# Optimization experiments

Hardware: AMD Instinct MI355X
Metric: run time of the kernel (lower is better)

Reference implementation:

```python
import jax, jax.numpy as jnp
import numpy as np

EPS = 1e-3

def setup_inputs() -> dict:
    key = jax.random.key(0)
    k1, k2 = jax.random.split(key)
    B, T, F, C = 8, 2048, 128, 32
    hidden_states = jax.random.normal(k1, (B, T, F, C), dtype=jnp.float32)
    scale = jnp.ones((C,), dtype=jnp.float32)
    return {"hidden_states": hidden_states, "scale": scale}


def reference(hidden_states, scale):
    # layout: [B, T, F, C]; cumulative group-norm over time axis=1,
    # stats reduced over feature+channel axes (2, 3).
    red_axes = (2, 3)
    x = hidden_states.astype(jnp.float32)

    # cumulative sum of values over time -> [B, T, 1, 1]
    sum_at_t = jnp.sum(x, axis=red_axes, keepdims=True)
    cum_sum = jnp.cumsum(sum_at_t, axis=1)

    # cumulative element counts (mask is all-ones)
    elems_at_t = jnp.full_like(sum_at_t, float(x.shape[2] * x.shape[3]))
    cum_count = jnp.cumsum(elems_at_t, axis=1)
    safe_count = jnp.maximum(cum_count, 1.0)

    cum_mean = cum_sum / safe_count                       # [B, T, 1, 1]

    sq_diff = jnp.square(x - cum_mean)                    # [B, T, F, C]
    cum_sq = jnp.cumsum(jnp.sum(sq_diff, axis=red_axes, keepdims=True), axis=1)
    cum_var = cum_sq / safe_count

    normalized = (x - cum_mean) * jax.lax.rsqrt(cum_var + EPS)
    normalized = normalized * scale.reshape(1, 1, 1, -1)  # per-channel affine
    return normalized.astype(hidden_states.dtype)
```

## Files before the change

kernel.cpp:

```cpp
#include <hip/hip_runtime.h>

#define B_DIM 8
#define T_DIM 2048
#define FC 4096
#define NSLAB (B_DIM * T_DIM)
#define EPS 1e-3f

__global__ __launch_bounds__(256) void stats_kernel(
    const float* __restrict__ x, float2* __restrict__ sq) {
  const int slab = blockIdx.x;
  const int tid = threadIdx.x;
  const float4* p = (const float4*)(x + (size_t)slab * FC);

  float s = 0.f, q = 0.f;
#pragma unroll
  for (int k = 0; k < 4; ++k) {
    float4 v = p[tid * 4 + k];
    s += v.x + v.y + v.z + v.w;
    q += v.x * v.x + v.y * v.y + v.z * v.z + v.w * v.w;
  }

#pragma unroll
  for (int off = 32; off >= 1; off >>= 1) {
    s += __shfl_down(s, off, 64);
    q += __shfl_down(q, off, 64);
  }
  __shared__ float ss[4], qq[4];
  const int lane = tid & 63, wave = tid >> 6;
  if (lane == 0) { ss[wave] = s; qq[wave] = q; }
  __syncthreads();
  if (tid == 0) {
    float2 r;
    r.x = ss[0] + ss[1] + ss[2] + ss[3];
    r.y = qq[0] + qq[1] + qq[2] + qq[3];
    sq[slab] = r;
  }
}

__device__ __forceinline__ float block_exscan256(float v) {
  const int lane = threadIdx.x & 63;
  const int wave = threadIdx.x >> 6;
  float x = v;
#pragma unroll
  for (int off = 1; off < 64; off <<= 1) {
    float y = __shfl_up(x, off, 64);
    if (lane >= off) x += y;
  }
  __shared__ float wtot[4];
  __syncthreads();
  if (lane == 63) wtot[wave] = x;
  __syncthreads();
  float wex = 0.f;
  for (int w = 0; w < wave; ++w) wex += wtot[w];
  return wex + x - v;
}

__global__ __launch_bounds__(256) void scan_kernel(
    const float2* __restrict__ sq, float2* __restrict__ mi) {
  const int b = blockIdx.x;
  const int tid = threadIdx.x;
  const int PER = T_DIM / 256;
  const float2* in = sq + (size_t)b * T_DIM;
  float2* out = mi + (size_t)b * T_DIM;
  const int t0 = tid * PER;

  float ls[8], lq[8];
#pragma unroll
  for (int j = 0; j < PER; ++j) {
    float2 v = in[t0 + j];
    ls[j] = v.x;
    lq[j] = v.y;
  }

  float acc = 0.f;
#pragma unroll
  for (int j = 0; j < PER; ++j) acc += ls[j];
  float excl = block_exscan256(acc);

  float mean[8], S2[8];
  float run = excl;
#pragma unroll
  for (int j = 0; j < PER; ++j) {
    run += ls[j];
    float cnt = (float)FC * (float)(t0 + j + 1);
    float m = run / cnt;
    mean[j] = m;
    S2[j] = lq[j] - 2.f * m * ls[j] + (float)FC * m * m;
  }

  float acc2 = 0.f;
#pragma unroll
  for (int j = 0; j < PER; ++j) acc2 += S2[j];
  float excl2 = block_exscan256(acc2);

  float run2 = excl2;
#pragma unroll
  for (int j = 0; j < PER; ++j) {
    run2 += S2[j];
    float cnt = (float)FC * (float)(t0 + j + 1);
    float var = run2 / cnt;
    float2 r;
    r.x = mean[j];
    r.y = rsqrtf(var + EPS);
    out[t0 + j] = r;
  }
}

__global__ __launch_bounds__(256) void norm_kernel(
    const float* __restrict__ x, const float2* __restrict__ mi,
    const float* __restrict__ scale, float* __restrict__ out) {
  const int slab = blockIdx.x;
  const int tid = threadIdx.x;
  const size_t base = (size_t)slab * FC;
  const float2 m = mi[slab];

  const float4* sp = (const float4*)(scale + ((tid * 16) & 31));
  float4 sc0 = sp[0], sc1 = sp[1], sc2 = sp[2], sc3 = sp[3];
  float4 scs[4] = {sc0, sc1, sc2, sc3};

  const float4* px = (const float4*)(x + base);
  float4* po = (float4*)(out + base);
#pragma unroll
  for (int k = 0; k < 4; ++k) {
    float4 v = px[tid * 4 + k];
    float4 s = scs[k];
    float4 r;
    r.x = (v.x - m.x) * m.y * s.x;
    r.y = (v.y - m.x) * m.y * s.y;
    r.z = (v.z - m.x) * m.y * s.z;
    r.w = (v.w - m.x) * m.y * s.w;
    po[tid * 4 + k] = r;
  }
}

extern "C" void kernel_launch(void* const* d_in, const int* in_sizes, int n_in,
                              void* d_out, int out_size, void* d_ws, size_t ws_size,
                              hipStream_t stream) {
  const float* x = (const float*)d_in[0];
  const float* scale = (const float*)d_in[1];
  float* out = (float*)d_out;

  float2* sq = (float2*)d_ws;
  float2* mi = sq + NSLAB;

  stats_kernel<<<NSLAB, 256, 0, stream>>>(x, sq);
  scan_kernel<<<B_DIM, 256, 0, stream>>>(sq, mi);
  norm_kernel<<<NSLAB, 256, 0, stream>>>(x, mi, scale, out);
}
```

Baseline: 502.0 us.

## Fuse stats, scan and normalize into single-pass decoupled-lookback kernel

Replaces the three-kernel pipeline (stats, per-batch scan, normalize) with one kernel. Each block takes a dynamic ticket, loads four time slabs into registers, and computes their sums. It then runs a decoupled-lookback prefix scan over per-group aggregates for both the mean and the variance terms, and normalizes from registers. This removes the second global read of the input and the intermediate launches. In exchange it adds spin-wait serialization along the time chain, relies on relaxed atomics for ordering, and raises register pressure from holding 16 float4 per thread.

```diff
diff --git a/kernel.cpp b/kernel.cpp
--- a/kernel.cpp
+++ b/kernel.cpp
@@ -1,135 +1,184 @@
 #include <hip/hip_runtime.h>
+
 
 #define B_DIM 8
 #define T_DIM 2048
 #define FC 4096
-#define NSLAB (B_DIM * T_DIM)
+#define SPB 4
+#define GPB (T_DIM / SPB)
+#define NGRP (B_DIM * GPB)
 #define EPS 1e-3f
 
-__global__ __launch_bounds__(256) void stats_kernel(
-    const float* __restrict__ x, float2* __restrict__ sq) {
-  const int slab = blockIdx.x;
+typedef unsigned long long u64;
+typedef unsigned int u32;
+
+struct Chain {
+  u64 a[NGRP];
+  u64 b[NGRP];
+  u32 ticket;
+};
+
+__global__ __launch_bounds__(256) void clear_kernel(Chain* __restrict__ ch) {
+  const int i = blockIdx.x * 256 + threadIdx.x;
+  if (i < NGRP) { ch->a[i] = 0ull; ch->b[i] = 0ull; }
+  if (i == 0) ch->ticket = 0u;
+}
+
+__device__ __forceinline__ u64 pack_entry(u32 st, float v) {
+  return ((u64)st << 32) | (u64)__float_as_uint(v);
+}
+
+__device__ __forceinline__ float lookback(u64* __restrict__ entry, int p, int lane) {
+  float pref = 0.f;
+  int j = p - 1;
+  while (j >= 0) {
+    const int idx = j - lane;
+    const bool valid = idx >= 0;
+    u64 e = valid ? __hip_atomic_load(&entry[idx], __ATOMIC_RELAXED,
+                                      __HIP_MEMORY_SCOPE_AGENT)
+                  : 0ull;
+    const u32 st = (u32)(e >> 32);
+    const u64 b2 = __ballot(valid && st == 2u);
+    const u64 b0 = __ballot(valid && st == 0u);
+    const int f2 = b2 ? (__ffsll(b2) - 1) : 64;
+    const int f0 = b0 ? (__ffsll(b0) - 1) : 64;
+    if (f0 < f2) {
+      __builtin_amdgcn_s_sleep(2);
+      continue;
+    }
+    float c = (valid && lane <= f2) ? __uint_as_float((u32)e) : 0.f;
+#pragma unroll
+    for (int o = 32; o >= 1; o >>= 1) c += __shfl_xor(c, o, 64);
+    pref += c;
+    if (f2 < 64) break;
+    j -= 64;
+  }
+  return pref;
+}
+
+__global__ __launch_bounds__(256, 4) void fused_kernel(
+    const float* __restrict__ x, const float* __restrict__ scale,
+    float* __restrict__ out, Chain* __restrict__ ch) {
+  __shared__ u32 s_vbid;
+  __shared__ float s_sq[4][8];
+  __shared__ float s_slab[8];
+  __shared__ float2 s_mi[SPB];
+
   const int tid = threadIdx.x;
-  const float4* p = (const float4*)(x + (size_t)slab * FC);
+  const int lane = tid & 63;
+  const int wave = tid >> 6;
 
-  float s = 0.f, q = 0.f;
+  if (tid == 0) s_vbid = atomicAdd(&ch->ticket, 1u);
+  __syncthreads();
+  const u32 vbid = s_vbid;
+  const int batch = vbid >> 9;
+  const int p = vbid & (GPB - 1);
+  const int t0 = p * SPB;
+
+  const size_t base = (size_t)(batch * T_DIM + t0) * FC;
+  const float4* px = (const float4*)(x + base);
+  float4 v[SPB][4];
+  float sj[SPB], qj[SPB];
 #pragma unroll
-  for (int k = 0; k < 4; ++k) {
-    float4 v = p[tid * 4 + k];
-    s += v.x + v.y + v.z + v.w;
-    q += v.x * v.x + v.y * v.y + v.z * v.z + v.w * v.w;
+  for (int j = 0; j < SPB; ++j) {
+    float s = 0.f, q = 0.f;
+#pragma unroll
+    for (int k = 0; k < 4; ++k) {
+      float4 t = px[j * 1024 + k * 256 + tid];
+      v[j][k] = t;
+      s += t.x + t.y + t.z + t.w;
+      q += t.x * t.x + t.y * t.y + t.z * t.z + t.w * t.w;
+    }
+    sj[j] = s;
+    qj[j] = q;
   }
 
 #pragma unroll
-  for (int off = 32; off >= 1; off >>= 1) {
-    s += __shfl_down(s, off, 64);
-    q += __shfl_down(q, off, 64);
+  for (int j = 0; j < SPB; ++j) {
+#pragma unroll
+    for (int o = 32; o >= 1; o >>= 1) {
+      sj[j] += __shfl_xor(sj[j], o, 64);
+      qj[j] += __shfl_xor(qj[j], o, 64);
+    }
   }
-  __shared__ float ss[4], qq[4];
-  const int lane = tid & 63, wave = tid >> 6;
-  if (lane == 0) { ss[wave] = s; qq[wave] = q; }
+  if (lane == 0) {
+#pragma unroll
+    for (int j = 0; j < SPB; ++j) {
+      s_sq[wave][j] = sj[j];
+      s_sq[wave][4 + j] = qj[j];
+    }
+  }
   __syncthreads();
-  if (tid == 0) {
-    float2 r;
-    r.x = ss[0] + ss[1] + ss[2] + ss[3];
-    r.y = qq[0] + qq[1] + qq[2] + qq[3];
-    sq[slab] = r;
+  if (tid < 8)
+    s_slab[tid] = s_sq[0][tid] + s_sq[1][tid] + s_sq[2][tid] + s_sq[3][tid];
+  __syncthreads();
+
+  if (wave == 0) {
+    float S[SPB], Q[SPB];
+#pragma unroll
+    for (int j = 0; j < SPB; ++j) {
+      S[j] = s_slab[j];
+      Q[j] = s_slab[4 + j];
+    }
+    u64* eA = ch->a + batch * GPB;
+    u64* eB = ch->b + batch * GPB;
+
+    const float aggS = S[0] + S[1] + S[2] + S[3];
+    if (p > 0 && lane == 0)
+      __hip_atomic_store(&eA[p], pack_entry(1u, aggS), __ATOMIC_RELAXED,
+                         __HIP_MEMORY_SCOPE_AGENT);
+    const float prefS = (p > 0) ? lookback(eA, p, lane) : 0.f;
+    if (lane == 0)
+      __hip_atomic_store(&eA[p], pack_entry(2u, prefS + aggS), __ATOMIC_RELAXED,
+                         __HIP_MEMORY_SCOPE_AGENT);
+
+    float m[SPB], S2[SPB];
+    float run = prefS;
+#pragma unroll
+    for (int j = 0; j < SPB; ++j) {
+      run += S[j];
+      const float cnt = (float)FC * (float)(t0 + j + 1);
+      m[j] = run / cnt;
+      S2[j] = Q[j] - 2.f * m[j] * S[j] + (float)FC * m[j] * m[j];
+    }
+
+    const float aggV = S2[0] + S2[1] + S2[2] + S2[3];
+    if (p > 0 && lane == 0)
+      __hip_atomic_store(&eB[p], pack_entry(1u, aggV), __ATOMIC_RELAXED,
+                         __HIP_MEMORY_SCOPE_AGENT);
+    const float prefV = (p > 0) ? lookback(eB, p, lane) : 0.f;
+    if (lane == 0) {
+      __hip_atomic_store(&eB[p], pack_entry(2u, prefV + aggV), __ATOMIC_RELAXED,
+                         __HIP_MEMORY_SCOPE_AGENT);
+      float r2 = prefV;
+#pragma unroll
+      for (int j = 0; j < SPB; ++j) {
+        r2 += S2[j];
+        const float cnt = (float)FC * (float)(t0 + j + 1);
+        float2 mi;
+        mi.x = m[j];
+        mi.y = rsqrtf(r2 / cnt + EPS);
+        s_mi[j] = mi;
+      }
+    }
   }
-}
+  __syncthreads();
 
-__device__ __forceinline__ float block_exscan256(float v) {
-  const int lane = threadIdx.x & 63;
-  const int wave = threadIdx.x >> 6;
-  float x = v;
-#pragma unroll
-  for (int off = 1; off < 64; off <<= 1) {
-    float y = __shfl_up(x, off, 64);
-    if (lane >= off) x += y;
-  }
-  __shared__ float wtot[4];
-  __syncthreads();
-  if (lane == 63) wtot[wave] = x;
-  __syncthreads();
-  float wex = 0.f;
-  for (int w = 0; w < wave; ++w) wex += wtot[w];
-  return wex + x - v;
-}
-
-__global__ __launch_bounds__(256) void scan_kernel(
-    const float2* __restrict__ sq, float2* __restrict__ mi) {
-  const int b = blockIdx.x;
-  const int tid = threadIdx.x;
-  const int PER = T_DIM / 256;
-  const float2* in = sq + (size_t)b * T_DIM;
-  float2* out = mi + (size_t)b * T_DIM;
-  const int t0 = tid * PER;
-
-  float ls[8], lq[8];
-#pragma unroll
-  for (int j = 0; j < PER; ++j) {
-    float2 v = in[t0 + j];
-    ls[j] = v.x;
-    lq[j] = v.y;
-  }
-
-  float acc = 0.f;
-#pragma unroll
-  for (int j = 0; j < PER; ++j) acc += ls[j];
-  float excl = block_exscan256(acc);
-
-  float mean[8], S2[8];
-  float run = excl;
-#pragma unroll
-  for (int j = 0; j < PER; ++j) {
-    run += ls[j];
-    float cnt = (float)FC * (float)(t0 + j + 1);
-    float m = run / cnt;
-    mean[j] = m;
-    S2[j] = lq[j] - 2.f * m * ls[j] + (float)FC * m * m;
-  }
-
-  float acc2 = 0.f;
-#pragma unroll
-  for (int j = 0; j < PER; ++j) acc2 += S2[j];
-  float excl2 = block_exscan256(acc2);
-
-  float run2 = excl2;
-#pragma unroll
-  for (int j = 0; j < PER; ++j) {
-    run2 += S2[j];
-    float cnt = (float)FC * (float)(t0 + j + 1);
-    float var = run2 / cnt;
-    float2 r;
-    r.x = mean[j];
-    r.y = rsqrtf(var + EPS);
-    out[t0 + j] = r;
-  }
-}
-
-__global__ __launch_bounds__(256) void norm_kernel(
-    const float* __restrict__ x, const float2* __restrict__ mi,
-    const float* __restrict__ scale, float* __restrict__ out) {
-  const int slab = blockIdx.x;
-  const int tid = threadIdx.x;
-  const size_t base = (size_t)slab * FC;
-  const float2 m = mi[slab];
-
-  const float4* sp = (const float4*)(scale + ((tid * 16) & 31));
-  float4 sc0 = sp[0], sc1 = sp[1], sc2 = sp[2], sc3 = sp[3];
-  float4 scs[4] = {sc0, sc1, sc2, sc3};
-
-  const float4* px = (const float4*)(x + base);
+  const float4 sc = *(const float4*)(scale + ((tid * 4) & 31));
   float4* po = (float4*)(out + base);
 #pragma unroll
-  for (int k = 0; k < 4; ++k) {
-    float4 v = px[tid * 4 + k];
-    float4 s = scs[k];
-    float4 r;
-    r.x = (v.x - m.x) * m.y * s.x;
-    r.y = (v.y - m.x) * m.y * s.y;
-    r.z = (v.z - m.x) * m.y * s.z;
-    r.w = (v.w - m.x) * m.y * s.w;
-    po[tid * 4 + k] = r;
+  for (int j = 0; j < SPB; ++j) {
+    const float2 mi = s_mi[j];
+#pragma unroll
+    for (int k = 0; k < 4; ++k) {
+      float4 t = v[j][k];
+      float4 r;
+      r.x = (t.x - mi.x) * mi.y * sc.x;
+      r.y = (t.y - mi.x) * mi.y * sc.y;
+      r.z = (t.z - mi.x) * mi.y * sc.z;
+      r.w = (t.w - mi.x) * mi.y * sc.w;
+      po[j * 1024 + k * 256 + tid] = r;
+    }
   }
 }
 
@@ -139,11 +188,8 @@
   const float* x = (const float*)d_in[0];
   const float* scale = (const float*)d_in[1];
   float* out = (float*)d_out;
+  Chain* ch = (Chain*)d_ws;
 
-  float2* sq = (float2*)d_ws;
-  float2* mi = sq + NSLAB;
-
-  stats_kernel<<<NSLAB, 256, 0, stream>>>(x, sq);
-  scan_kernel<<<B_DIM, 256, 0, stream>>>(sq, mi);
-  norm_kernel<<<NSLAB, 256, 0, stream>>>(x, mi, scale, out);
+  clear_kernel<<<(NGRP + 255) / 256, 256, 0, stream>>>(ch);
+  fused_kernel<<<NGRP, 256, 0, stream>>>(x, scale, out, ch);
 }
```

Measured after the change: 477.9 us. 1.05x faster.
